# Performance work log

Hardware: AMD Instinct MI355X
Metric: run time of the kernel (lower is better)

Reference implementation:

```python
import jax, jax.numpy as jnp
import numpy as np

N = 500_000
LEVELS = 3
GDIM = 8
BASE_H = 128
BASE_W = 128
COND = 64
DOUT = 128
HID = 2
DIN = 1 + 2 * LEVELS * GDIM  # rho + theta-grid feats + rho-grid feats = 49


def _bilinear(grid, u, v):
    # grid: [H, W, D]; u, v in [0,1]; u indexes W axis, v indexes H axis.
    H, W, D = grid.shape
    x = u * (W - 1)
    y = v * (H - 1)
    x0 = jnp.clip(jnp.floor(x).astype(jnp.int32), 0, W - 2)
    y0 = jnp.clip(jnp.floor(y).astype(jnp.int32), 0, H - 2)
    x1 = x0 + 1
    y1 = y0 + 1
    wx = (x - x0)[:, None]
    wy = (y - y0)[:, None]
    g = grid.reshape(H * W, D)
    c00 = jnp.take(g, y0 * W + x0, axis=0)
    c01 = jnp.take(g, y0 * W + x1, axis=0)
    c10 = jnp.take(g, y1 * W + x0, axis=0)
    c11 = jnp.take(g, y1 * W + x1, axis=0)
    return (c00 * (1 - wx) * (1 - wy) + c01 * wx * (1 - wy)
            + c10 * (1 - wx) * wy + c11 * wx * wy)


def setup_inputs() -> dict:
    key = jax.random.key(0)
    ks = jax.random.split(key, 24)
    inp = {
        'coords': jax.random.uniform(ks[0], (N,), dtype=jnp.float32),
        'angles': jax.random.uniform(ks[1], (N,), dtype=jnp.float32),
        'rho': jax.random.normal(ks[2], (N,), dtype=jnp.float32),
        'rho_n': jax.random.uniform(ks[3], (N,), dtype=jnp.float32),
        'curve_feats': jax.random.normal(ks[4], (N, COND), dtype=jnp.float32),
        'type_sample': jax.random.normal(ks[5], (N, DOUT), dtype=jnp.float32),
    }
    # Multi-resolution grids (theta-conditioned and rho-conditioned).
    for l in range(LEVELS):
        h, w = BASE_H * 2 ** l, BASE_W * 2 ** l
        inp[f'gt{l}'] = 0.1 * jax.random.normal(ks[6 + l], (h, w, GDIM), dtype=jnp.float32)
        inp[f'gr{l}'] = 0.1 * jax.random.normal(ks[9 + l], (h, w, GDIM), dtype=jnp.float32)
    # FiLM-modulated encoder chain (block 0 + HID residual blocks).
    inp['film0_fcW'] = jax.random.normal(ks[12], (DIN, DOUT), dtype=jnp.float32) / np.sqrt(DIN)
    inp['film0_fcb'] = jnp.zeros((DOUT,), dtype=jnp.float32)
    inp['filmh_fcW'] = jax.random.normal(ks[13], (HID, DOUT, DOUT), dtype=jnp.float32) / np.sqrt(DOUT)
    inp['filmh_fcb'] = jnp.zeros((HID, DOUT), dtype=jnp.float32)
    inp['gammaW'] = 0.02 * jax.random.normal(ks[14], (HID + 1, COND, DOUT), dtype=jnp.float32)
    inp['gammab'] = jnp.ones((HID + 1, DOUT), dtype=jnp.float32)
    inp['betaW'] = 0.02 * jax.random.normal(ks[15], (HID + 1, COND, DOUT), dtype=jnp.float32)
    inp['betab'] = jnp.zeros((HID + 1, DOUT), dtype=jnp.float32)
    # Decoder MLP [DOUT, 64, 1].
    inp['decW1'] = jax.random.normal(ks[16], (DOUT, 64), dtype=jnp.float32) / np.sqrt(DOUT)
    inp['decb1'] = jnp.zeros((64,), dtype=jnp.float32)
    inp['decW2'] = jax.random.normal(ks[17], (64, 1), dtype=jnp.float32) / 8.0
    inp['decb2'] = jnp.zeros((1,), dtype=jnp.float32)
    return inp


def reference(coords, angles, rho, rho_n, curve_feats, type_sample,
              gt0, gt1, gt2, gr0, gr1, gr2,
              film0_fcW, film0_fcb, filmh_fcW, filmh_fcb,
              gammaW, gammab, betaW, betab,
              decW1, decb1, decW2, decb2):
    # Multi-res grid interpolation, concat across levels.
    ct = jnp.concatenate([_bilinear(g, angles, coords) for g in (gt0, gt1, gt2)], axis=-1)
    cr = jnp.concatenate([_bilinear(g, rho_n, coords) for g in (gr0, gr1, gr2)], axis=-1)
    feat = jnp.concatenate([rho[:, None], ct, cr], axis=-1)  # [N, DIN]
    # FiLM conditioning: gamma/beta per block from curve_feats.
    gamma = jnp.einsum('nc,lcd->lnd', curve_feats, gammaW) + gammab[:, None, :]
    beta = jnp.einsum('nc,lcd->lnd', curve_feats, betaW) + betab[:, None, :]
    # Block 0 + type_sample residual.
    x = jax.nn.silu(gamma[0] * (feat @ film0_fcW + film0_fcb) + beta[0]) + type_sample
    # Residual FiLM blocks.
    for i in range(filmh_fcW.shape[0]):
        x = x + jax.nn.silu(gamma[i + 1] * (x @ filmh_fcW[i] + filmh_fcb[i]) + beta[i + 1])
    # Decoder MLP.
    h = jax.nn.relu(x @ decW1 + decb1)
    sdf = (h @ decW2 + decb2)[..., 0]  # [N]
    return sdf
```

## Files before the change

kernel.cpp:

```cpp
#include <hip/hip_runtime.h>
#include <stdint.h>

typedef short s16x8 __attribute__((ext_vector_type(8)));
typedef float f32x4 __attribute__((ext_vector_type(4)));
typedef uint32_t u32x4 __attribute__((ext_vector_type(4)));

#define MFMA16(a, b, c) __builtin_amdgcn_mfma_f32_16x16x32_bf16(a, b, c, 0, 0, 0)

__device__ __forceinline__ short f2bf(float f) {
  uint32_t u = __builtin_bit_cast(uint32_t, f);
  u += 0x7FFFu + ((u >> 16) & 1u);
  return (short)(u >> 16);
}
__device__ __forceinline__ uint32_t cvtpk(float lo, float hi) {
  uint32_t r;
  asm("v_cvt_pk_bf16_f32 %0, %1, %2" : "=v"(r) : "v"(lo), "v"(hi));
  return r;
}
__device__ __forceinline__ short f2bf1(float f) { return (short)cvtpk(f, f); }

__global__ void pack_w(const float* __restrict__ w0, const float* __restrict__ wh,
                       const float* __restrict__ gw, const float* __restrict__ bw,
                       const float* __restrict__ d1, short* __restrict__ out) {
  int idx = blockIdx.x * 512 + threadIdx.x;
  if (idx >= 98304) return;
  int f = idx >> 9;
  int r = idx & 511;
  int lane = r >> 3, e = r & 7;
  int kk = ((lane >> 4) << 3) + e;
  int nn = lane & 15;
  float v;
  if (f < 16) {
    int ct = f >> 1, ks = f & 1;
    int k = ks * 32 + kk, n = ct * 16 + nn;
    if (k < 48) v = w0[(1 + k) * 128 + n];
    else if (k == 48) v = w0[n];
    else v = 0.f;
  } else if (f < 112) {
    int f2 = f - 16;
    int ks = f2 & 1, ct = (f2 >> 1) & 7, gb = (f2 >> 4) & 1, l = f2 >> 5;
    int k = ks * 32 + kk, n = ct * 16 + nn;
    const float* Wp = gb ? bw : gw;
    v = Wp[(l * 64 + k) * 128 + n];
  } else if (f < 176) {
    int f2 = f - 112;
    int ks = f2 & 3, ct = (f2 >> 2) & 7, i = f2 >> 5;
    int k = ks * 32 + kk, n = ct * 16 + nn;
    v = wh[(i * 128 + k) * 128 + n];
  } else {
    int f2 = f - 176;
    int ks = f2 & 3, ct = f2 >> 2;
    int k = ks * 32 + kk, n = ct * 16 + nn;
    v = d1[k * 64 + n];
  }
  out[idx] = f2bf(v);
}

__global__ __launch_bounds__(512) void ngc_gather(
    const float* __restrict__ coords, const float* __restrict__ angles,
    const float* __restrict__ rho, const float* __restrict__ rho_n,
    const float* __restrict__ gt0, const float* __restrict__ gr0,
    const float* __restrict__ gt1, const float* __restrict__ gr1,
    const float* __restrict__ gt2, const float* __restrict__ gr2,
    short* __restrict__ stage, int n, int t0) {
  const int tid = threadIdx.x;
  const int row0 = (t0 + blockIdx.x) * 64;
  char* st = (char*)(stage + (size_t)blockIdx.x * 4096);

  if (tid < 384) {
    int r = tid & 63, g = tid >> 6;
    int gr_ = row0 + r; gr_ = gr_ < n ? gr_ : n - 1;
    float vv = coords[gr_];
    float u = (g < 3) ? angles[gr_] : rho_n[gr_];
    int lvl = (g < 3) ? g : g - 3;
    const float* G = (g == 0) ? gt0 : (g == 1) ? gt1 : (g == 2) ? gt2
                   : (g == 3) ? gr0 : (g == 4) ? gr1 : gr2;
    int Wg = 128 << lvl;
    float x = u * (float)(Wg - 1), y = vv * (float)(Wg - 1);
    int ix = (int)x; ix = ix < 0 ? 0 : (ix > Wg - 2 ? Wg - 2 : ix);
    int iy = (int)y; iy = iy < 0 ? 0 : (iy > Wg - 2 ? Wg - 2 : iy);
    float wx = x - (float)ix, wy = y - (float)iy;
    const float4* p0 = (const float4*)(G + (size_t)(iy * Wg + ix) * 8);
    const float4* p1 = (const float4*)(G + (size_t)((iy + 1) * Wg + ix) * 8);
    float4 c00a = p0[0], c00b = p0[1], c01a = p0[2], c01b = p0[3];
    float4 c10a = p1[0], c10b = p1[1], c11a = p1[2], c11b = p1[3];
    float w00 = (1.f - wx) * (1.f - wy), w01 = wx * (1.f - wy);
    float w10 = (1.f - wx) * wy, w11 = wx * wy;
    float e0 = c00a.x * w00 + c01a.x * w01 + c10a.x * w10 + c11a.x * w11;
    float e1 = c00a.y * w00 + c01a.y * w01 + c10a.y * w10 + c11a.y * w11;
    float e2 = c00a.z * w00 + c01a.z * w01 + c10a.z * w10 + c11a.z * w11;
    float e3 = c00a.w * w00 + c01a.w * w01 + c10a.w * w10 + c11a.w * w11;
    float e4 = c00b.x * w00 + c01b.x * w01 + c10b.x * w10 + c11b.x * w11;
    float e5 = c00b.y * w00 + c01b.y * w01 + c10b.y * w10 + c11b.y * w11;
    float e6 = c00b.z * w00 + c01b.z * w01 + c10b.z * w10 + c11b.z * w11;
    float e7 = c00b.w * w00 + c01b.w * w01 + c10b.w * w10 + c11b.w * w11;
    u32x4 o = { cvtpk(e0, e1), cvtpk(e2, e3), cvtpk(e4, e5), cvtpk(e6, e7) };
    int dst16 = ((r >> 4) * 2 + (g >> 2)) * 64 + (g & 3) * 16 + (r & 15);
    *(u32x4*)(st + dst16 * 16) = o;
  } else if (tid < 448) {
    int r = tid - 384;
    int gr_ = row0 + r; gr_ = gr_ < n ? gr_ : n - 1;
    s16x8 a = { f2bf1(rho[gr_]), 0, 0, 0, 0, 0, 0, 0 };
    int base = ((r >> 4) * 2 + 1) * 64;
    *(s16x8*)(st + (base + 32 + (r & 15)) * 16) = a;
  } else {
    int r = tid - 448;
    s16x8 z = { 0, 0, 0, 0, 0, 0, 0, 0 };
    int base = ((r >> 4) * 2 + 1) * 64;
    *(s16x8*)(st + (base + 48 + (r & 15)) * 16) = z;
  }
}

__global__ __launch_bounds__(512) void ngc_gemm(
    const float* __restrict__ cf, const float* __restrict__ ts,
    const float* __restrict__ f0b, const float* __restrict__ fhb,
    const float* __restrict__ gab, const float* __restrict__ beb,
    const float* __restrict__ d1b, const float* __restrict__ d2w,
    const float* __restrict__ d2b, const short* __restrict__ pw,
    const short* __restrict__ stage, float* __restrict__ out, int n, int t0) {
  __shared__ __align__(16) char smem[25 * 1024];
  char* cfA = smem;
  char* xA  = smem + 8 * 1024;
  float* red = (float*)(smem + 24 * 1024);

  const int tid = threadIdx.x;
  const int lane = tid & 63;
  const int w = tid >> 6;
  const int g16 = lane >> 4;
  const int l15 = lane & 15;
  const int row0 = (t0 + blockIdx.x) * 64;
  const int col = w * 16 + l15;
  const int cbase = col >> 5;
  const int cslot = ((col >> 3) & 3) * 16;
  const int ce = (col & 7) * 2;

  float tsr[4][4];
#pragma unroll
  for (int rg = 0; rg < 4; ++rg)
#pragma unroll
    for (int rr = 0; rr < 4; ++rr) {
      int grow = row0 + rg * 16 + g16 * 4 + rr; grow = grow < n ? grow : n - 1;
      tsr[rg][rr] = ts[(size_t)grow * 128 + col];
    }

  {
    int cb = tid & 7, r = tid >> 3;
    int gr_ = row0 + r; gr_ = gr_ < n ? gr_ : n - 1;
    const float4* cp = (const float4*)(cf + (size_t)gr_ * 64 + cb * 8);
    float4 v0 = cp[0], v1 = cp[1];
    u32x4 s = { cvtpk(v0.x, v0.y), cvtpk(v0.z, v0.w),
                cvtpk(v1.x, v1.y), cvtpk(v1.z, v1.w) };
    int dst16 = ((r >> 4) * 2 + (cb >> 2)) * 64 + (cb & 3) * 16 + (r & 15);
    *(u32x4*)(cfA + dst16 * 16) = s;
  }
  __syncthreads();

  const s16x8* fB = (const s16x8*)stage + (size_t)blockIdx.x * 512;
  auto ldfeat = [&](int frag) -> s16x8 { return fB[frag * 64 + lane]; };
  auto ldF = [&](const char* b, int frag) -> s16x8 {
    return *(const s16x8*)(b + (frag * 64 + lane) * 16);
  };
  auto ldw = [&](int frag) -> s16x8 { return ((const s16x8*)pw)[frag * 64 + lane]; };

  float xr[4][4];

  {
    s16x8 bw0 = ldw(w * 2), bw1 = ldw(w * 2 + 1);
    s16x8 bg0 = ldw(16 + w * 2), bg1 = ldw(16 + w * 2 + 1);
    s16x8 bb0 = ldw(32 + w * 2), bb1 = ldw(32 + w * 2 + 1);
    float f0bv = f0b[col], gabv = gab[col], bebv = beb[col];
#pragma unroll
    for (int rg = 0; rg < 4; ++rg) {
      s16x8 a0 = ldfeat(rg * 2), a1 = ldfeat(rg * 2 + 1);
      s16x8 c0 = ldF(cfA, rg * 2), c1 = ldF(cfA, rg * 2 + 1);
      f32x4 t = {0.f, 0.f, 0.f, 0.f};
      t = MFMA16(a0, bw0, t); t = MFMA16(a1, bw1, t);
      f32x4 ga = {0.f, 0.f, 0.f, 0.f};
      ga = MFMA16(c0, bg0, ga); ga = MFMA16(c1, bg1, ga);
      f32x4 be = {0.f, 0.f, 0.f, 0.f};
      be = MFMA16(c0, bb0, be); be = MFMA16(c1, bb1, be);
      char* xbase = xA + (rg * 4 + cbase) * 1024 + ce;
#pragma unroll
      for (int rr = 0; rr < 4; ++rr) {
        float z = (ga[rr] + gabv) * (t[rr] + f0bv) + (be[rr] + bebv);
        float sl = z * __builtin_amdgcn_rcpf(1.f + __expf(-z));
        xr[rg][rr] = sl + tsr[rg][rr];
        *(short*)(xbase + (cslot + g16 * 4 + rr) * 16) = f2bf1(xr[rg][rr]);
      }
    }
  }
  __syncthreads();

#pragma unroll
  for (int i = 0; i < 2; ++i) {
    s16x8 bh0 = ldw(112 + i * 32 + w * 4);
    s16x8 bh1 = ldw(112 + i * 32 + w * 4 + 1);
    s16x8 bh2 = ldw(112 + i * 32 + w * 4 + 2);
    s16x8 bh3 = ldw(112 + i * 32 + w * 4 + 3);
    s16x8 bg0 = ldw(16 + (i + 1) * 32 + w * 2);
    s16x8 bg1 = ldw(16 + (i + 1) * 32 + w * 2 + 1);
    s16x8 bb0 = ldw(16 + (i + 1) * 32 + 16 + w * 2);
    s16x8 bb1 = ldw(16 + (i + 1) * 32 + 16 + w * 2 + 1);
    float fhbv = fhb[i * 128 + col];
    float gabv = gab[(i + 1) * 128 + col];
    float bebv = beb[(i + 1) * 128 + col];
    f32x4 zs[4];
#pragma unroll
    for (int rg = 0; rg < 4; ++rg) {
      s16x8 xa = ldF(xA, rg * 4), xb = ldF(xA, rg * 4 + 1);
      s16x8 xc = ldF(xA, rg * 4 + 2), xd = ldF(xA, rg * 4 + 3);
      s16x8 c0 = ldF(cfA, rg * 2), c1 = ldF(cfA, rg * 2 + 1);
      f32x4 t = {0.f, 0.f, 0.f, 0.f};
      t = MFMA16(xa, bh0, t); t = MFMA16(xb, bh1, t);
      t = MFMA16(xc, bh2, t); t = MFMA16(xd, bh3, t);
      f32x4 ga = {0.f, 0.f, 0.f, 0.f};
      ga = MFMA16(c0, bg0, ga); ga = MFMA16(c1, bg1, ga);
      f32x4 be = {0.f, 0.f, 0.f, 0.f};
      be = MFMA16(c0, bb0, be); be = MFMA16(c1, bb1, be);
      f32x4 z;
#pragma unroll
      for (int rr = 0; rr < 4; ++rr) {
        float zz = (ga[rr] + gabv) * (t[rr] + fhbv) + (be[rr] + bebv);
        z[rr] = zz * __builtin_amdgcn_rcpf(1.f + __expf(-zz));
      }
      zs[rg] = z;
    }
    __syncthreads();
#pragma unroll
    for (int rg = 0; rg < 4; ++rg) {
      char* xbase = xA + (rg * 4 + cbase) * 1024 + ce;
#pragma unroll
      for (int rr = 0; rr < 4; ++rr) {
        xr[rg][rr] += zs[rg][rr];
        *(short*)(xbase + (cslot + g16 * 4 + rr) * 16) = f2bf1(xr[rg][rr]);
      }
    }
    __syncthreads();
  }

  {
    int ctd = w & 3, rbase = (w >> 2) * 2;
    int dcol = ctd * 16 + l15;
    s16x8 bd0 = ldw(176 + ctd * 4), bd1 = ldw(176 + ctd * 4 + 1);
    s16x8 bd2 = ldw(176 + ctd * 4 + 2), bd3 = ldw(176 + ctd * 4 + 3);
    float d1bv = d1b[dcol], w2v = d2w[dcol];
#pragma unroll
    for (int q = 0; q < 2; ++q) {
      int rg = rbase + q;
      s16x8 xa = ldF(xA, rg * 4), xb = ldF(xA, rg * 4 + 1);
      s16x8 xc = ldF(xA, rg * 4 + 2), xd = ldF(xA, rg * 4 + 3);
      f32x4 hh = {0.f, 0.f, 0.f, 0.f};
      hh = MFMA16(xa, bd0, hh); hh = MFMA16(xb, bd1, hh);
      hh = MFMA16(xc, bd2, hh); hh = MFMA16(xd, bd3, hh);
#pragma unroll
      for (int rr = 0; rr < 4; ++rr) {
        float h = fmaxf(hh[rr] + d1bv, 0.f) * w2v;
        h += __shfl_xor(h, 1);
        h += __shfl_xor(h, 2);
        h += __shfl_xor(h, 4);
        h += __shfl_xor(h, 8);
        if (l15 == 0) red[(rg * 16 + g16 * 4 + rr) * 4 + ctd] = h;
      }
    }
  }
  __syncthreads();
  if (tid < 64) {
    int grow = row0 + tid;
    if (grow < n)
      out[grow] = red[tid * 4 + 0] + red[tid * 4 + 1] + red[tid * 4 + 2] +
                  red[tid * 4 + 3] + d2b[0];
  }
}

extern "C" void kernel_launch(void* const* d_in, const int* in_sizes, int n_in,
                              void* d_out, int out_size, void* d_ws, size_t ws_size,
                              hipStream_t stream) {
  int n = in_sizes[0];
  short* pw = (short*)d_ws;
  const size_t stage_off = 256 * 1024;
  short* stage = (short*)((char*)d_ws + stage_off);
  int ntiles = (n + 63) / 64;
  long long avail = (long long)ws_size - (long long)stage_off;
  int chunk = (int)(avail > 8192 ? avail / 8192 : 1);
  if (chunk > ntiles) chunk = ntiles;
  if (chunk < 1) chunk = 1;

  pack_w<<<192, 512, 0, stream>>>(
      (const float*)d_in[12],
      (const float*)d_in[14],
      (const float*)d_in[16],
      (const float*)d_in[18],
      (const float*)d_in[20],
      pw);

  for (int t0 = 0; t0 < ntiles; t0 += chunk) {
    int nb = ntiles - t0 < chunk ? ntiles - t0 : chunk;
    ngc_gather<<<nb, 512, 0, stream>>>(
        (const float*)d_in[0],
        (const float*)d_in[1],
        (const float*)d_in[2],
        (const float*)d_in[3],
        (const float*)d_in[6],
        (const float*)d_in[7],
        (const float*)d_in[8],
        (const float*)d_in[9],
        (const float*)d_in[10],
        (const float*)d_in[11],
        stage, n, t0);
    ngc_gemm<<<nb, 512, 0, stream>>>(
        (const float*)d_in[4],
        (const float*)d_in[5],
        (const float*)d_in[13],
        (const float*)d_in[15],
        (const float*)d_in[17],
        (const float*)d_in[19],
        (const float*)d_in[21],
        (const float*)d_in[22],
        (const float*)d_in[23],
        pw, stage, (float*)d_out, n, t0);
  }
}
```

Baseline: 284.5 us.

## Ping-pong x buffers in shared memory and restructure decoder as transposed MFMA

Double-buffers the activation tile in shared memory so each residual block reads one buffer and writes the other, removing the mid-block barrier and the zs register staging. The decoder now runs on four waves with a transposed MFMA (weights as A, activations as B), so each lane accumulates its own row's output with only two cross-lane shuffles. This drops the shared reduction array and the final barrier. Decoder bias and second-layer weights are pre-permuted into a lane-matched float layout by pack_w. Shared memory grows from 25 KB to 40 KB, which may lower occupancy, and half the waves sit idle during the decoder.

```diff
diff --git a/kernel.cpp b/kernel.cpp
--- a/kernel.cpp
+++ b/kernel.cpp
@@ -21,39 +21,49 @@
 
 __global__ void pack_w(const float* __restrict__ w0, const float* __restrict__ wh,
                        const float* __restrict__ gw, const float* __restrict__ bw,
-                       const float* __restrict__ d1, short* __restrict__ out) {
+                       const float* __restrict__ d1, const float* __restrict__ d1bp,
+                       const float* __restrict__ d2wp, short* __restrict__ out,
+                       float* __restrict__ dpk) {
   int idx = blockIdx.x * 512 + threadIdx.x;
-  if (idx >= 98304) return;
-  int f = idx >> 9;
-  int r = idx & 511;
-  int lane = r >> 3, e = r & 7;
-  int kk = ((lane >> 4) << 3) + e;
-  int nn = lane & 15;
-  float v;
-  if (f < 16) {
-    int ct = f >> 1, ks = f & 1;
-    int k = ks * 32 + kk, n = ct * 16 + nn;
-    if (k < 48) v = w0[(1 + k) * 128 + n];
-    else if (k == 48) v = w0[n];
-    else v = 0.f;
-  } else if (f < 112) {
-    int f2 = f - 16;
-    int ks = f2 & 1, ct = (f2 >> 1) & 7, gb = (f2 >> 4) & 1, l = f2 >> 5;
-    int k = ks * 32 + kk, n = ct * 16 + nn;
-    const float* Wp = gb ? bw : gw;
-    v = Wp[(l * 64 + k) * 128 + n];
-  } else if (f < 176) {
-    int f2 = f - 112;
-    int ks = f2 & 3, ct = (f2 >> 2) & 7, i = f2 >> 5;
-    int k = ks * 32 + kk, n = ct * 16 + nn;
-    v = wh[(i * 128 + k) * 128 + n];
-  } else {
-    int f2 = f - 176;
-    int ks = f2 & 3, ct = f2 >> 2;
-    int k = ks * 32 + kk, n = ct * 16 + nn;
-    v = d1[k * 64 + n];
-  }
-  out[idx] = f2bf(v);
+  if (idx < 98304) {
+    int f = idx >> 9;
+    int r = idx & 511;
+    int lane = r >> 3, e = r & 7;
+    int kk = ((lane >> 4) << 3) + e;
+    int nn = lane & 15;
+    float v;
+    if (f < 16) {
+      int ct = f >> 1, ks = f & 1;
+      int k = ks * 32 + kk, n = ct * 16 + nn;
+      if (k < 48) v = w0[(1 + k) * 128 + n];
+      else if (k == 48) v = w0[n];
+      else v = 0.f;
+    } else if (f < 112) {
+      int f2 = f - 16;
+      int ks = f2 & 1, ct = (f2 >> 1) & 7, gb = (f2 >> 4) & 1, l = f2 >> 5;
+      int k = ks * 32 + kk, n = ct * 16 + nn;
+      const float* Wp = gb ? bw : gw;
+      v = Wp[(l * 64 + k) * 128 + n];
+    } else if (f < 176) {
+      int f2 = f - 112;
+      int ks = f2 & 3, ct = (f2 >> 2) & 7, i = f2 >> 5;
+      int k = ks * 32 + kk, n = ct * 16 + nn;
+      v = wh[(i * 128 + k) * 128 + n];
+    } else {
+      int f2 = f - 176;
+      int ks = f2 & 3, ct = f2 >> 2;
+      int k = ks * 32 + kk, n = ct * 16 + nn;
+      v = d1[k * 64 + n];
+    }
+    out[idx] = f2bf(v);
+  } else if (idx < 100352) {
+    int j = idx - 98304;
+    int which = j >> 10;
+    int k = j & 1023;
+    int ct = k >> 8, lane = (k >> 2) & 63, rr = k & 3;
+    int n2 = ct * 16 + ((lane >> 4) << 2) + rr;
+    dpk[j] = which ? d2wp[n2] : d1bp[n2];
+  }
 }
 
 __global__ __launch_bounds__(512) void ngc_gather(
@@ -115,13 +125,13 @@
     const float* __restrict__ cf, const float* __restrict__ ts,
     const float* __restrict__ f0b, const float* __restrict__ fhb,
     const float* __restrict__ gab, const float* __restrict__ beb,
-    const float* __restrict__ d1b, const float* __restrict__ d2w,
     const float* __restrict__ d2b, const short* __restrict__ pw,
-    const short* __restrict__ stage, float* __restrict__ out, int n, int t0) {
-  __shared__ __align__(16) char smem[25 * 1024];
+    const float* __restrict__ dpk, const short* __restrict__ stage,
+    float* __restrict__ out, int n, int t0) {
+  __shared__ __align__(16) char smem[40 * 1024];
   char* cfA = smem;
-  char* xA  = smem + 8 * 1024;
-  float* red = (float*)(smem + 24 * 1024);
+  char* x0  = smem + 8 * 1024;
+  char* x1  = smem + 24 * 1024;
 
   const int tid = threadIdx.x;
   const int lane = tid & 63;
@@ -134,6 +144,8 @@
   const int cslot = ((col >> 3) & 3) * 16;
   const int ce = (col & 7) * 2;
 
+  const float d2b0 = d2b[0];
+
   float tsr[4][4];
 #pragma unroll
   for (int rg = 0; rg < 4; ++rg)
@@ -179,7 +191,7 @@
       ga = MFMA16(c0, bg0, ga); ga = MFMA16(c1, bg1, ga);
       f32x4 be = {0.f, 0.f, 0.f, 0.f};
       be = MFMA16(c0, bb0, be); be = MFMA16(c1, bb1, be);
-      char* xbase = xA + (rg * 4 + cbase) * 1024 + ce;
+      char* xbase = x0 + (rg * 4 + cbase) * 1024 + ce;
 #pragma unroll
       for (int rr = 0; rr < 4; ++rr) {
         float z = (ga[rr] + gabv) * (t[rr] + f0bv) + (be[rr] + bebv);
@@ -193,6 +205,8 @@
 
 #pragma unroll
   for (int i = 0; i < 2; ++i) {
+    const char* xsrc = i ? x1 : x0;
+    char* xdst = i ? x0 : x1;
     s16x8 bh0 = ldw(112 + i * 32 + w * 4);
     s16x8 bh1 = ldw(112 + i * 32 + w * 4 + 1);
     s16x8 bh2 = ldw(112 + i * 32 + w * 4 + 2);
@@ -204,11 +218,10 @@
     float fhbv = fhb[i * 128 + col];
     float gabv = gab[(i + 1) * 128 + col];
     float bebv = beb[(i + 1) * 128 + col];
-    f32x4 zs[4];
 #pragma unroll
     for (int rg = 0; rg < 4; ++rg) {
-      s16x8 xa = ldF(xA, rg * 4), xb = ldF(xA, rg * 4 + 1);
-      s16x8 xc = ldF(xA, rg * 4 + 2), xd = ldF(xA, rg * 4 + 3);
+      s16x8 xa = ldF(xsrc, rg * 4), xb = ldF(xsrc, rg * 4 + 1);
+      s16x8 xc = ldF(xsrc, rg * 4 + 2), xd = ldF(xsrc, rg * 4 + 3);
       s16x8 c0 = ldF(cfA, rg * 2), c1 = ldF(cfA, rg * 2 + 1);
       f32x4 t = {0.f, 0.f, 0.f, 0.f};
       t = MFMA16(xa, bh0, t); t = MFMA16(xb, bh1, t);
@@ -217,58 +230,41 @@
       ga = MFMA16(c0, bg0, ga); ga = MFMA16(c1, bg1, ga);
       f32x4 be = {0.f, 0.f, 0.f, 0.f};
       be = MFMA16(c0, bb0, be); be = MFMA16(c1, bb1, be);
-      f32x4 z;
+      char* xbase = xdst + (rg * 4 + cbase) * 1024 + ce;
 #pragma unroll
       for (int rr = 0; rr < 4; ++rr) {
         float zz = (ga[rr] + gabv) * (t[rr] + fhbv) + (be[rr] + bebv);
-        z[rr] = zz * __builtin_amdgcn_rcpf(1.f + __expf(-zz));
-      }
-      zs[rg] = z;
-    }
-    __syncthreads();
-#pragma unroll
-    for (int rg = 0; rg < 4; ++rg) {
-      char* xbase = xA + (rg * 4 + cbase) * 1024 + ce;
-#pragma unroll
-      for (int rr = 0; rr < 4; ++rr) {
-        xr[rg][rr] += zs[rg][rr];
+        xr[rg][rr] += zz * __builtin_amdgcn_rcpf(1.f + __expf(-zz));
         *(short*)(xbase + (cslot + g16 * 4 + rr) * 16) = f2bf1(xr[rg][rr]);
       }
     }
     __syncthreads();
   }
 
-  {
-    int ctd = w & 3, rbase = (w >> 2) * 2;
-    int dcol = ctd * 16 + l15;
-    s16x8 bd0 = ldw(176 + ctd * 4), bd1 = ldw(176 + ctd * 4 + 1);
-    s16x8 bd2 = ldw(176 + ctd * 4 + 2), bd3 = ldw(176 + ctd * 4 + 3);
-    float d1bv = d1b[dcol], w2v = d2w[dcol];
-#pragma unroll
-    for (int q = 0; q < 2; ++q) {
-      int rg = rbase + q;
-      s16x8 xa = ldF(xA, rg * 4), xb = ldF(xA, rg * 4 + 1);
-      s16x8 xc = ldF(xA, rg * 4 + 2), xd = ldF(xA, rg * 4 + 3);
+  if (w < 4) {
+    const int rg = w;
+    s16x8 xF0 = ldF(x0, rg * 4), xF1 = ldF(x0, rg * 4 + 1);
+    s16x8 xF2 = ldF(x0, rg * 4 + 2), xF3 = ldF(x0, rg * 4 + 3);
+    float s = 0.f;
+#pragma unroll
+    for (int ct = 0; ct < 4; ++ct) {
       f32x4 hh = {0.f, 0.f, 0.f, 0.f};
-      hh = MFMA16(xa, bd0, hh); hh = MFMA16(xb, bd1, hh);
-      hh = MFMA16(xc, bd2, hh); hh = MFMA16(xd, bd3, hh);
-#pragma unroll
-      for (int rr = 0; rr < 4; ++rr) {
-        float h = fmaxf(hh[rr] + d1bv, 0.f) * w2v;
-        h += __shfl_xor(h, 1);
-        h += __shfl_xor(h, 2);
-        h += __shfl_xor(h, 4);
-        h += __shfl_xor(h, 8);
-        if (l15 == 0) red[(rg * 16 + g16 * 4 + rr) * 4 + ctd] = h;
-      }
-    }
-  }
-  __syncthreads();
-  if (tid < 64) {
-    int grow = row0 + tid;
-    if (grow < n)
-      out[grow] = red[tid * 4 + 0] + red[tid * 4 + 1] + red[tid * 4 + 2] +
-                  red[tid * 4 + 3] + d2b[0];
+      hh = MFMA16(ldw(176 + ct * 4 + 0), xF0, hh);
+      hh = MFMA16(ldw(176 + ct * 4 + 1), xF1, hh);
+      hh = MFMA16(ldw(176 + ct * 4 + 2), xF2, hh);
+      hh = MFMA16(ldw(176 + ct * 4 + 3), xF3, hh);
+      f32x4 db = *(const f32x4*)&dpk[ct * 256 + lane * 4];
+      f32x4 wv = *(const f32x4*)&dpk[1024 + ct * 256 + lane * 4];
+#pragma unroll
+      for (int rr = 0; rr < 4; ++rr)
+        s += fmaxf(hh[rr] + db[rr], 0.f) * wv[rr];
+    }
+    s += __shfl_xor(s, 16);
+    s += __shfl_xor(s, 32);
+    if (g16 == 0) {
+      int grow = row0 + rg * 16 + l15;
+      if (grow < n) out[grow] = s + d2b0;
+    }
   }
 }
 
@@ -277,6 +273,7 @@
                               hipStream_t stream) {
   int n = in_sizes[0];
   short* pw = (short*)d_ws;
+  float* dpk = (float*)((char*)d_ws + 192 * 1024);
   const size_t stage_off = 256 * 1024;
   short* stage = (short*)((char*)d_ws + stage_off);
   int ntiles = (n + 63) / 64;
@@ -285,13 +282,15 @@
   if (chunk > ntiles) chunk = ntiles;
   if (chunk < 1) chunk = 1;
 
-  pack_w<<<192, 512, 0, stream>>>(
+  pack_w<<<196, 512, 0, stream>>>(
       (const float*)d_in[12],
       (const float*)d_in[14],
       (const float*)d_in[16],
       (const float*)d_in[18],
       (const float*)d_in[20],
-      pw);
+      (const float*)d_in[21],
+      (const float*)d_in[22],
+      pw, dpk);
 
   for (int t0 = 0; t0 < ntiles; t0 += chunk) {
     int nb = ntiles - t0 < chunk ? ntiles - t0 : chunk;
@@ -314,9 +313,7 @@
         (const float*)d_in[15],
         (const float*)d_in[17],
         (const float*)d_in[19],
-        (const float*)d_in[21],
-        (const float*)d_in[22],
         (const float*)d_in[23],
-        pw, stage, (float*)d_out, n, t0);
-  }
-}
+        pw, dpk, stage, (float*)d_out, n, t0);
+  }
+}
```

Result: faster. 271.5 us (-4.6%).
